# Kernel optimization log

Measured on AMD Instinct MI355X. Metric: run time of the kernel, lower is better.

The kernel has to match this reference:

```python
import jax, jax.numpy as jnp
import numpy as np

G, D, H = 64, 16, 8   # n groups, per-group input dim, GRU hidden (feat_dim)
B, T = 64, 512


def setup_inputs() -> dict:
    key = jax.random.key(0)
    ks = jax.random.split(key, 5)
    s = 1.0 / np.sqrt(H)  # PyTorch GRU init: U(-1/sqrt(hidden), 1/sqrt(hidden))
    x = jax.random.normal(ks[0], (B, T, G * D), dtype=jnp.float32)
    W_ih = jax.random.uniform(ks[1], (G, 3 * H, D), jnp.float32, -s, s)
    W_hh = jax.random.uniform(ks[2], (G, 3 * H, H), jnp.float32, -s, s)
    b_ih = jax.random.uniform(ks[3], (G, 3 * H), jnp.float32, -s, s)
    b_hh = jax.random.uniform(ks[4], (G, 3 * H), jnp.float32, -s, s)
    return {"x": x, "W_ih": W_ih, "W_hh": W_hh, "b_ih": b_ih, "b_hh": b_hh}


def reference(x, W_ih, W_hh, b_ih, b_hh):
    # x: [B, T, G*D] -> per-group GRU, output [B, T, G, H]
    Bq, Tq, _ = x.shape
    xg = x.reshape(Bq, Tq, G, D)
    # Precompute all input-to-hidden gate projections as one grouped GEMM.
    gx = jnp.einsum('btgd,gkd->btgk', xg, W_ih) + b_ih  # [B, T, G, 3H]
    gx = jnp.moveaxis(gx, 1, 0)                          # [T, B, G, 3H]
    h0 = jnp.zeros((Bq, G, H), dtype=x.dtype)

    def step(h, gxt):
        gh = jnp.einsum('bgh,gkh->bgk', h, W_hh) + b_hh  # [B, G, 3H]
        xr, xz, xn = jnp.split(gxt, 3, axis=-1)          # PyTorch gate order: r, z, n
        hr, hz, hn = jnp.split(gh, 3, axis=-1)
        r = jax.nn.sigmoid(xr + hr)
        z = jax.nn.sigmoid(xz + hz)
        n = jnp.tanh(xn + r * hn)
        h_new = (1.0 - z) * n + z * h
        return h_new, h_new

    _, hs = jax.lax.scan(step, h0, gx)  # hs: [T, B, G, H]
    return jnp.moveaxis(hs, 0, 1)       # [B, T, G, H]
```

## Files before the change

kernel.cpp:

```cpp
#include <hip/hip_runtime.h>


#define Gn 64
#define Dn 16
#define Hn 8
#define Tn 512

typedef float v2f __attribute__((ext_vector_type(2)));

__device__ __forceinline__ float rcp_fast(float v) { return __builtin_amdgcn_rcpf(v); }
__device__ __forceinline__ float exp2_fast(float v) { return __builtin_amdgcn_exp2f(v); }

#define KNL (-1.44269504088896340736f)
#define KP2 ( 2.88539008177792681472f)

template <int CTRL>
__device__ __forceinline__ float dppf(float v) {
    return __int_as_float(
        __builtin_amdgcn_update_dpp(0, __float_as_int(v), CTRL, 0xF, 0xF, false));
}

__global__ __attribute__((amdgpu_flat_work_group_size(64, 64),
                          amdgpu_waves_per_eu(1, 1)))
void mcgru_kernel(
    const float* __restrict__ x,
    const float* __restrict__ W_ih,
    const float* __restrict__ W_hh,
    const float* __restrict__ b_ih,
    const float* __restrict__ b_hh,
    float* __restrict__ out)
{
    const int tid  = blockIdx.x * blockDim.x + threadIdx.x;
    const int cell = tid >> 3;
    const int l    = tid & 7;
    const int g    = cell & (Gn - 1);
    const int b    = cell >> 6;
    const int s4   = l & 3;
    const int q    = l >> 2;

    int jmap[8];
#pragma unroll
    for (int k = 0; k < 8; ++k) {
        const int hi2 = k >> 2, r = k & 3;
        jmap[k] = ((q ^ hi2) << 2) | (s4 ^ r ^ (hi2 ? 3 : 0));
    }

    const float scale[3] = {KNL, KNL, KP2};

    v2f   wih[3][8];
    float whh[3][8];
    float bs[3];
    float bhn;
#pragma unroll
    for (int qg = 0; qg < 3; ++qg) {
        const int row = qg * Hn + l;
        const float sc = scale[qg];
        const float4* wr = (const float4*)(W_ih + ((size_t)g * 24 + row) * Dn);
#pragma unroll
        for (int i = 0; i < 4; ++i) {
            float4 v = wr[i];
            wih[qg][2*i+0] = (v2f){v.x * sc, v.y * sc};
            wih[qg][2*i+1] = (v2f){v.z * sc, v.w * sc};
        }
        const float* hrow = W_hh + ((size_t)g * 24 + row) * Hn;
#pragma unroll
        for (int k = 0; k < 8; ++k) whh[qg][k] = hrow[jmap[k]] * sc;
        if (qg < 2) {
            bs[qg] = (b_ih[g * 24 + row] + b_hh[g * 24 + row]) * sc;
        } else {
            bs[qg] = b_ih[g * 24 + row] * sc;
            bhn    = b_hh[g * 24 + row] * sc;
        }
    }
#pragma unroll
    for (int qg = 0; qg < 3; ++qg) {
#pragma unroll
        for (int i = 0; i < 8; ++i) asm volatile("" : "+v"(wih[qg][i]));
#pragma unroll
        for (int k = 0; k < 8; ++k) asm volatile("" : "+v"(whh[qg][k]));
        asm volatile("" : "+v"(bs[qg]));
    }
    asm volatile("" : "+v"(bhn));

    const float* xp = x   + ((size_t)b * Tn * Gn + g) * Dn;
    float*       op = out + ((size_t)b * Tn * Gn + g) * Hn + l;

    auto load_x = [&](int t, v2f* xv) {
        const float4* p = (const float4*)(xp + (size_t)t * Gn * Dn);
#pragma unroll
        for (int i = 0; i < 4; ++i) {
            float4 v = p[i];
            xv[2*i+0] = (v2f){v.x, v.y};
            xv[2*i+1] = (v2f){v.z, v.w};
        }
    };
    auto proj = [&](const v2f* xv, float* gx) {
#pragma unroll
        for (int qg = 0; qg < 3; ++qg) {
            v2f acc = wih[qg][0] * xv[0];
#pragma unroll
            for (int i = 1; i < 8; ++i) acc += wih[qg][i] * xv[i];
            gx[qg] = (bs[qg] + acc.x) + acc.y;
        }
    };

    float h = 0.0f;
    auto step = [&](const float* gx, int t) {
        float H[8];
        H[0] = h;
        H[1] = dppf<0xB1>(h);
        H[2] = dppf<0x4E>(h);
        H[3] = dppf<0x1B>(h);
        H[4] = dppf<0x141>(H[0]);
        H[5] = dppf<0x141>(H[1]);
        H[6] = dppf<0x141>(H[2]);
        H[7] = dppf<0x141>(H[3]);

        float gh[3];
#pragma unroll
        for (int qg = 0; qg < 3; ++qg) {
            float a = fmaf(whh[qg][1], H[1], whh[qg][0] * H[0]);
            a = fmaf(whh[qg][2], H[2], a);
            a = fmaf(whh[qg][3], H[3], a);
            float c = (qg == 2) ? fmaf(whh[qg][4], H[4], bhn)
                                : whh[qg][4] * H[4];
            c = fmaf(whh[qg][5], H[5], c);
            c = fmaf(whh[qg][6], H[6], c);
            c = fmaf(whh[qg][7], H[7], c);
            gh[qg] = a + c;
        }
        const float r  = rcp_fast(1.0f + exp2_fast(gx[0] + gh[0]));
        const float z  = rcp_fast(1.0f + exp2_fast(gx[1] + gh[1]));
        const float zh = z * h;
        const float om = 1.0f - z;
        const float e  = exp2_fast(fmaf(r, gh[2], gx[2]));
        const float n  = fmaf(-2.0f, rcp_fast(e + 1.0f), 1.0f);
        h = fmaf(n, om, zh);
        __builtin_nontemporal_store(h, op + (size_t)t * (Gn * Hn));
    };

    v2f   xv[8][8];
    float gx[4][3];

    {
        v2f t0[8], t1[8];
        load_x(0, t0);
        load_x(1, t1);
        load_x(2, xv[2]); load_x(3, xv[3]); load_x(4, xv[4]);
        load_x(5, xv[5]); load_x(6, xv[6]); load_x(7, xv[7]);
        proj(t0, gx[0]);
        proj(t1, gx[1]);
    }

    for (int t = 0; t < Tn; t += 8) {
#pragma unroll
        for (int j = 0; j < 8; ++j) {
            const int s = t + j;
            int tl = s + 8; if (tl > Tn - 1) tl = Tn - 1;
            v2f* slot = xv[(j + 2) & 7];
            asm volatile("" : "+v"(slot[0]), "+v"(slot[1]), "+v"(slot[2]),
                              "+v"(slot[3]), "+v"(slot[4]), "+v"(slot[5]),
                              "+v"(slot[6]), "+v"(slot[7]));
            load_x(tl, xv[j]);
            proj(slot, gx[(j + 2) & 3]);
            step(gx[j & 3], s);
        }
    }
}

extern "C" void kernel_launch(void* const* d_in, const int* in_sizes, int n_in,
                              void* d_out, int out_size, void* d_ws, size_t ws_size,
                              hipStream_t stream) {
    const float* x    = (const float*)d_in[0];
    const float* W_ih = (const float*)d_in[1];
    const float* W_hh = (const float*)d_in[2];
    const float* b_ih = (const float*)d_in[3];
    const float* b_hh = (const float*)d_in[4];
    float* out = (float*)d_out;

    dim3 grid(512), block(64);
    hipLaunchKernelGGL(mcgru_kernel, grid, block, 0, stream,
                       x, W_ih, W_hh, b_ih, b_hh, out);
}
```

Baseline: 278.2 us.

## Split x loads across lanes and share via DPP in input projection

Each of the 8 lanes of a cell now loads only its own 2-float slice of the 16-float input row instead of all 16 floats, and the full row is rebuilt with DPP cross-lane moves inside the projection. W_ih columns are permuted with the same lane map to match. This cuts redundant global load traffic and the registers needed for the 8-deep prefetch ring by 8x. In exchange it adds 14 DPP ops per timestep onto the ALU path and makes each load narrower.

```diff
diff --git a/kernel.cpp b/kernel.cpp
--- a/kernel.cpp
+++ b/kernel.cpp
@@ -18,6 +18,13 @@
 __device__ __forceinline__ float dppf(float v) {
     return __int_as_float(
         __builtin_amdgcn_update_dpp(0, __float_as_int(v), CTRL, 0xF, 0xF, false));
+}
+template <int CTRL>
+__device__ __forceinline__ v2f dpp2(v2f v) {
+    v2f r;
+    r.x = dppf<CTRL>(v.x);
+    r.y = dppf<CTRL>(v.y);
+    return r;
 }
 
 __global__ __attribute__((amdgpu_flat_work_group_size(64, 64),
@@ -55,12 +62,11 @@
     for (int qg = 0; qg < 3; ++qg) {
         const int row = qg * Hn + l;
         const float sc = scale[qg];
-        const float4* wr = (const float4*)(W_ih + ((size_t)g * 24 + row) * Dn);
+        const float* wr = W_ih + ((size_t)g * 24 + row) * Dn;
 #pragma unroll
-        for (int i = 0; i < 4; ++i) {
-            float4 v = wr[i];
-            wih[qg][2*i+0] = (v2f){v.x * sc, v.y * sc};
-            wih[qg][2*i+1] = (v2f){v.z * sc, v.w * sc};
+        for (int k = 0; k < 8; ++k) {
+            const int dp = jmap[k] * 2;
+            wih[qg][k] = (v2f){wr[dp] * sc, wr[dp + 1] * sc};
         }
         const float* hrow = W_hh + ((size_t)g * 24 + row) * Hn;
 #pragma unroll
@@ -82,24 +88,27 @@
     }
     asm volatile("" : "+v"(bhn));
 
-    const float* xp = x   + ((size_t)b * Tn * Gn + g) * Dn;
+    const float* xq = x   + ((size_t)b * Tn * Gn + g) * Dn + 2 * l;
     float*       op = out + ((size_t)b * Tn * Gn + g) * Hn + l;
 
-    auto load_x = [&](int t, v2f* xv) {
-        const float4* p = (const float4*)(xp + (size_t)t * Gn * Dn);
-#pragma unroll
-        for (int i = 0; i < 4; ++i) {
-            float4 v = p[i];
-            xv[2*i+0] = (v2f){v.x, v.y};
-            xv[2*i+1] = (v2f){v.z, v.w};
-        }
+    auto load_x = [&](int t) -> v2f {
+        return *(const v2f*)(xq + (size_t)t * (Gn * Dn));
     };
-    auto proj = [&](const v2f* xv, float* gx) {
+    auto proj = [&](v2f xv, float* gx) {
+        v2f X[8];
+        X[0] = xv;
+        X[1] = dpp2<0xB1>(xv);
+        X[2] = dpp2<0x4E>(xv);
+        X[3] = dpp2<0x1B>(xv);
+        X[4] = dpp2<0x141>(X[0]);
+        X[5] = dpp2<0x141>(X[1]);
+        X[6] = dpp2<0x141>(X[2]);
+        X[7] = dpp2<0x141>(X[3]);
 #pragma unroll
         for (int qg = 0; qg < 3; ++qg) {
-            v2f acc = wih[qg][0] * xv[0];
+            v2f acc = wih[qg][0] * X[0];
 #pragma unroll
-            for (int i = 1; i < 8; ++i) acc += wih[qg][i] * xv[i];
+            for (int i = 1; i < 8; ++i) acc += wih[qg][i] * X[i];
             gx[qg] = (bs[qg] + acc.x) + acc.y;
         }
     };
@@ -139,15 +148,14 @@
         __builtin_nontemporal_store(h, op + (size_t)t * (Gn * Hn));
     };
 
-    v2f   xv[8][8];
+    v2f   xr[8];
     float gx[4][3];
 
     {
-        v2f t0[8], t1[8];
-        load_x(0, t0);
-        load_x(1, t1);
-        load_x(2, xv[2]); load_x(3, xv[3]); load_x(4, xv[4]);
-        load_x(5, xv[5]); load_x(6, xv[6]); load_x(7, xv[7]);
+        v2f t0 = load_x(0);
+        v2f t1 = load_x(1);
+        xr[2] = load_x(2); xr[3] = load_x(3); xr[4] = load_x(4);
+        xr[5] = load_x(5); xr[6] = load_x(6); xr[7] = load_x(7);
         proj(t0, gx[0]);
         proj(t1, gx[1]);
     }
@@ -157,12 +165,9 @@
         for (int j = 0; j < 8; ++j) {
             const int s = t + j;
             int tl = s + 8; if (tl > Tn - 1) tl = Tn - 1;
-            v2f* slot = xv[(j + 2) & 7];
-            asm volatile("" : "+v"(slot[0]), "+v"(slot[1]), "+v"(slot[2]),
-                              "+v"(slot[3]), "+v"(slot[4]), "+v"(slot[5]),
-                              "+v"(slot[6]), "+v"(slot[7]));
-            load_x(tl, xv[j]);
-            proj(slot, gx[(j + 2) & 3]);
+            xr[j] = load_x(tl);
+            asm volatile("" : "+v"(xr[(j + 2) & 7]));
+            proj(xr[(j + 2) & 7], gx[(j + 2) & 3]);
             step(gx[j & 3], s);
         }
     }
```

Measured after the change: 289.2 us. +4.0%, slower.
